# Kernel tuning notes

Hardware: AMD Instinct MI355X
Metric: run time of the kernel (lower is better)

The kernel has to match this reference:

```python
import jax, jax.numpy as jnp
import numpy as np

N_NODES = 50000
N_GRAPHS = 16
NEG_SLOPE = 0.2


def gat_layer(x, W, a_s, a_d, b, src, dst, num_nodes):
    # h: [N, out]
    h = x @ W
    # per-node attention logits (heads=1)
    al_s = (h * a_s).sum(-1)  # [N]
    al_d = (h * a_d).sum(-1)  # [N]
    e = jax.nn.leaky_relu(al_s[src] + al_d[dst], NEG_SLOPE)  # [E]
    # segment softmax over incoming edges of each destination node
    m = jax.ops.segment_max(e, dst, num_segments=num_nodes)
    p = jnp.exp(e - m[dst])
    z = jax.ops.segment_sum(p, dst, num_segments=num_nodes)
    coef = p / z[dst]  # self-loops guarantee z > 0
    out = jax.ops.segment_sum(coef[:, None] * h[src], dst, num_segments=num_nodes)
    return out + b


def setup_inputs() -> dict:
    key = jax.random.key(0)
    ks = jax.random.split(key, 20)
    in_dim, hid, out_dim = 256, 128, 128
    E = 800000
    x = jax.random.normal(ks[0], (N_NODES, in_dim), dtype=jnp.float32)
    edge_index = jax.random.randint(ks[1], (2, E), 0, N_NODES, dtype=jnp.int32)
    batch = jnp.sort(jax.random.randint(ks[2], (N_NODES,), 0, N_GRAPHS, dtype=jnp.int32))

    def glorot(k, shape):
        fan = shape[0] + shape[-1]
        s = jnp.sqrt(6.0 / fan)
        return jax.random.uniform(k, shape, jnp.float32, -s, s)

    dims = [(in_dim, hid), (hid, hid), (hid, out_dim)]
    inp = {"x": x, "edge_index": edge_index, "batch": batch}
    for i, (di, do) in enumerate(dims):
        inp[f"W{i}"] = glorot(ks[3 + 4 * i], (di, do))
        inp[f"as{i}"] = glorot(ks[4 + 4 * i], (1, do))[0]
        inp[f"ad{i}"] = glorot(ks[5 + 4 * i], (1, do))[0]
        inp[f"b{i}"] = jnp.zeros((do,), jnp.float32)
    return inp


def reference(x, edge_index, batch, W0, as0, ad0, b0, W1, as1, ad1, b1, W2, as2, ad2, b2):
    # add self loops once (PyG GATConv add_self_loops=True)
    loops = jnp.arange(N_NODES, dtype=edge_index.dtype)
    src = jnp.concatenate([edge_index[0], loops])
    dst = jnp.concatenate([edge_index[1], loops])

    h = gat_layer(x, W0, as0, ad0, b0, src, dst, N_NODES)
    h = jax.nn.relu(h)  # act; dropout is identity at eval
    h = gat_layer(h, W1, as1, ad1, b1, src, dst, N_NODES)
    h = jax.nn.relu(h)
    node_emb = gat_layer(h, W2, as2, ad2, b2, src, dst, N_NODES)

    # global_mean_pool
    b32 = batch.astype(jnp.int32)
    sums = jax.ops.segment_sum(node_emb, b32, num_segments=N_GRAPHS)
    cnt = jax.ops.segment_sum(jnp.ones((N_NODES,), node_emb.dtype), b32, num_segments=N_GRAPHS)
    return sums / jnp.maximum(cnt, 1.0)[:, None]
```

## Files before the change

### kernel.cpp

```cpp
#include <hip/hip_runtime.h>
#include <math.h>

#define NN 50000
#define NE 800000
#define NTE (NE + NN)
#define NG 16
#define HID 128
#define NEG_SLOPE 0.2f

#define NBUK 391
#define SLOT 2560
#define EPW 4096
#define NWG_E ((NTE + EPW - 1) / EPW)
#define GEMM_GRID ((NN + 63) / 64)

#define BPAD 136
#define SMEM_BYTES 34816

typedef __attribute__((ext_vector_type(8))) __bf16 bf16x8;
typedef __attribute__((ext_vector_type(4))) float f32x4;

union V16 {
    float4 f4;
    uint4 u4;
    bf16x8 b8;
    __bf16 h[8];
};

__global__ void k_prep(int* __restrict__ bwr, float* __restrict__ sums,
                       int* __restrict__ off,
                       const float* __restrict__ W0, const float* __restrict__ W1,
                       const float* __restrict__ W2, __bf16* __restrict__ Wt0,
                       __bf16* __restrict__ Wt1, __bf16* __restrict__ Wt2) {
    int t = blockIdx.x * blockDim.x + threadIdx.x;
    if (t == 0) off[NN] = NTE;
    if (t <= NBUK) bwr[t] = 0;
    if (t < NG * HID) sums[t] = 0.0f;
    if (t < 256 * HID) {
        int k = t >> 7, n = t & 127;
        Wt0[(size_t)n * 256 + k] = (__bf16)W0[t];
    } else if (t < 256 * HID + HID * HID) {
        int u = t - 256 * HID;
        int k = u >> 7, n = u & 127;
        Wt1[(size_t)n * HID + k] = (__bf16)W1[u];
    } else if (t < 256 * HID + 2 * HID * HID) {
        int u = t - 256 * HID - HID * HID;
        int k = u >> 7, n = u & 127;
        Wt2[(size_t)n * HID + k] = (__bf16)W2[u];
    }
}

__device__ __forceinline__ void scatter_body(const int* __restrict__ ei,
                                             int* __restrict__ bwr,
                                             int* __restrict__ rec, int blk,
                                             char* smem) {
    int* hist = (int*)smem;
    int* cur = hist + NBUK;
    int t = threadIdx.x;
    for (int b = t; b < NBUK; b += 256) hist[b] = 0;
    __syncthreads();
    int base = blk * EPW;
    #pragma unroll
    for (int r = 0; r < EPW / 256; r++) {
        int idx = base + r * 256 + t;
        if (idx < NTE) {
            int dst = (idx < NE) ? ei[NE + idx] : (idx - NE);
            atomicAdd(&hist[dst >> 7], 1);
        }
    }
    __syncthreads();
    for (int b = t; b < NBUK; b += 256) {
        int c = hist[b];
        if (c) cur[b] = atomicAdd(&bwr[b], c);
    }
    __syncthreads();
    #pragma unroll
    for (int r = 0; r < EPW / 256; r++) {
        int idx = base + r * 256 + t;
        if (idx < NTE) {
            int src, dst;
            if (idx < NE) { src = ei[idx]; dst = ei[NE + idx]; }
            else          { src = idx - NE; dst = src; }
            int b = dst >> 7;
            int pos = atomicAdd(&cur[b], 1);
            rec[(size_t)b * SLOT + pos] = src | ((dst & 127) << 17);
        }
    }
}

__device__ __forceinline__ void scan512(const int* __restrict__ bwr, int* s) {
    int t = threadIdx.x;
    s[t] = (t < NBUK) ? bwr[t] : 0;
    s[t + 256] = (t + 256 < NBUK) ? bwr[t + 256] : 0;
    __syncthreads();
    for (int o = 1; o < 512; o <<= 1) {
        int a0 = (t >= o) ? s[t - o] : 0;
        int a1 = s[t + 256 - o];
        __syncthreads();
        s[t] += a0;
        s[t + 256] += a1;
        __syncthreads();
    }
}

__global__ __launch_bounds__(256) void k_bfill(const int* __restrict__ bwr,
                                               const int* __restrict__ rec,
                                               int* __restrict__ off,
                                               int* __restrict__ csr) {
    __shared__ int s[512];
    __shared__ int cnt[128];
    __shared__ int scn[128];
    __shared__ int cur[128];
    int b = blockIdx.x, t = threadIdx.x;
    scan512(bwr, s);
    int base = s[b] - bwr[b];
    int n = bwr[b];
    const int* rb = rec + (size_t)b * SLOT;
    if (t < 128) cnt[t] = 0;
    __syncthreads();
    for (int i = t; i < n; i += 256) atomicAdd(&cnt[rb[i] >> 17], 1);
    __syncthreads();
    if (t < 128) scn[t] = cnt[t];
    __syncthreads();
    #pragma unroll
    for (int o = 1; o < 128; o <<= 1) {
        int add = (t >= o && t < 128) ? scn[t - o] : 0;
        __syncthreads();
        if (t < 128) scn[t] += add;
        __syncthreads();
    }
    if (t < 128) {
        int ex = scn[t] - cnt[t];
        cur[t] = ex;
        int d = b * 128 + t;
        if (d < NN) off[d] = base + ex;
    }
    __syncthreads();
    for (int i = t; i < n; i += 256) {
        int r = rb[i];
        int dloc = r >> 17;
        int src = r & 131071;
        int pos = atomicAdd(&cur[dloc], 1);
        csr[base + pos] = src;
    }
}

template <typename AT, int K>
__device__ __forceinline__ void gemm_body(const AT* __restrict__ A,
                                          const __bf16* __restrict__ Bt,
                                          __bf16* __restrict__ C,
                                          const float* __restrict__ a_s,
                                          const float* __restrict__ a_d,
                                          float* __restrict__ als,
                                          float* __restrict__ ald,
                                          int M, int blk, char* smem) {
    __bf16(*Bs)[BPAD] = (__bf16(*)[BPAD])smem;

    int tid = threadIdx.x;
    int rowBase = blk * 64;
    int wv = tid >> 6;
    int lane = tid & 63;
    int g = lane >> 4;
    int c = lane & 15;

    int rowA = rowBase + wv * 16 + c;
    bool va = rowA < M;

    f32x4 acc[8];
    #pragma unroll
    for (int ni = 0; ni < 8; ni++) acc[ni] = (f32x4){0.f, 0.f, 0.f, 0.f};

    for (int kh = 0; kh < K; kh += 128) {
        if (kh) __syncthreads();
        #pragma unroll
        for (int rep = 0; rep < 8; rep++) {
            int ch = rep * 256 + tid;
            int r = ch >> 4, q = ch & 15;
            *(float4*)&Bs[r][q * 8] = *(const float4*)(Bt + (size_t)r * K + kh + q * 8);
        }
        bf16x8 afr[4];
        #pragma unroll
        for (int kc = 0; kc < 4; kc++) {
            if constexpr (sizeof(AT) == 2) {
                V16 t;
                t.f4 = (float4){0.f, 0.f, 0.f, 0.f};
                if (va) t.f4 = *(const float4*)((const __bf16*)A + (size_t)rowA * K + kh + kc * 32 + g * 8);
                afr[kc] = t.b8;
            } else {
                float vv[8] = {0.f, 0.f, 0.f, 0.f, 0.f, 0.f, 0.f, 0.f};
                if (va) {
                    const float* Ap = (const float*)A + (size_t)rowA * K + kh + kc * 32 + g * 8;
                    float4 v0 = *(const float4*)Ap;
                    float4 v1 = *(const float4*)(Ap + 4);
                    vv[0] = v0.x; vv[1] = v0.y; vv[2] = v0.z; vv[3] = v0.w;
                    vv[4] = v1.x; vv[5] = v1.y; vv[6] = v1.z; vv[7] = v1.w;
                }
                V16 t;
                #pragma unroll
                for (int q = 0; q < 8; q++) t.h[q] = (__bf16)vv[q];
                afr[kc] = t.b8;
            }
        }
        __syncthreads();

        #pragma unroll
        for (int kc = 0; kc < 4; kc++) {
            #pragma unroll
            for (int ni = 0; ni < 8; ni++) {
                bf16x8 b = *(const bf16x8*)&Bs[ni * 16 + c][kc * 32 + g * 8];
                acc[ni] = __builtin_amdgcn_mfma_f32_16x16x32_bf16(afr[kc], b, acc[ni], 0, 0, 0);
            }
        }
    }

    float asv[8], adv[8];
    #pragma unroll
    for (int ni = 0; ni < 8; ni++) {
        asv[ni] = a_s[ni * 16 + c];
        adv[ni] = a_d[ni * 16 + c];
    }
    int rb = rowBase + wv * 16 + g * 4;
    #pragma unroll
    for (int i = 0; i < 4; i++) {
        int row = rb + i;
        float s = 0.f, dd = 0.f;
        #pragma unroll
        for (int ni = 0; ni < 8; ni++) {
            float v = acc[ni][i];
            s = fmaf(v, asv[ni], s);
            dd = fmaf(v, adv[ni], dd);
        }
        #pragma unroll
        for (int o = 1; o <= 8; o <<= 1) {
            s += __shfl_xor(s, o);
            dd += __shfl_xor(dd, o);
        }
        if (row < M) {
            #pragma unroll
            for (int ni = 0; ni < 8; ni++)
                C[(size_t)row * HID + ni * 16 + c] = (__bf16)acc[ni][i];
            if (c == 0) {
                als[row] = s;
                ald[row] = dd;
            }
        }
    }
}

__global__ __launch_bounds__(256, 4) void k_gemm_bf16(const __bf16* __restrict__ A,
                                                      const __bf16* __restrict__ Bt,
                                                      __bf16* __restrict__ C,
                                                      const float* __restrict__ a_s,
                                                      const float* __restrict__ a_d,
                                                      float* __restrict__ als,
                                                      float* __restrict__ ald) {
    __shared__ __align__(16) char smem[SMEM_BYTES];
    gemm_body<__bf16, HID>(A, Bt, C, a_s, a_d, als, ald, NN, blockIdx.x, smem);
}

__global__ __launch_bounds__(256, 4) void k_gemm0_scatter(const float* __restrict__ x,
                                                          const __bf16* __restrict__ Wt0,
                                                          __bf16* __restrict__ C,
                                                          const float* __restrict__ a_s,
                                                          const float* __restrict__ a_d,
                                                          float* __restrict__ als,
                                                          float* __restrict__ ald,
                                                          const int* __restrict__ ei,
                                                          int* __restrict__ bwr,
                                                          int* __restrict__ rec) {
    __shared__ __align__(16) char smem[SMEM_BYTES];
    if (blockIdx.x < GEMM_GRID) {
        gemm_body<float, 256>(x, Wt0, C, a_s, a_d, als, ald, NN, blockIdx.x, smem);
    } else {
        scatter_body(ei, bwr, rec, blockIdx.x - GEMM_GRID, smem);
    }
}

__global__ __launch_bounds__(256) void k_attn(const __bf16* __restrict__ h,
                                              const float* __restrict__ als,
                                              const float* __restrict__ ald,
                                              const int* __restrict__ off,
                                              const int* __restrict__ csr,
                                              const float* __restrict__ bias,
                                              __bf16* __restrict__ yout,
                                              int do_relu) {
    __shared__ int2 s_e[4][64];
    int gt = blockIdx.x * blockDim.x + threadIdx.x;
    int d = gt >> 6;
    int lane = gt & 63;
    if (d >= NN) return;
    int wv = threadIdx.x >> 6;
    int grp = lane >> 4;
    int c = lane & 15;

    int e0 = off[d], e1 = off[d + 1];
    int deg = e1 - e0;
    float ald_d = ald[d];
    float acc[8] = {0.f, 0.f, 0.f, 0.f, 0.f, 0.f, 0.f, 0.f};

    if (deg <= 64) {
        int s = 0;
        float e = -INFINITY;
        if (lane < deg) {
            s = csr[e0 + lane];
            float t = als[s] + ald_d;
            e = (t > 0.0f) ? t : NEG_SLOPE * t;
        }
        float mx = e;
        #pragma unroll
        for (int o = 32; o > 0; o >>= 1) mx = fmaxf(mx, __shfl_xor(mx, o));
        float p = (lane < deg) ? __expf(e - mx) : 0.0f;
        float z = p;
        #pragma unroll
        for (int o = 32; o > 0; o >>= 1) z += __shfl_xor(z, o);
        float inv_z = 1.0f / z;
        s_e[wv][lane] = make_int2(s, __float_as_int(p * inv_z));

        int degR = (deg + 3) & ~3;
        #pragma unroll 4
        for (int k = grp; k < degR; k += 4) {
            int2 pr = s_e[wv][k];
            int ss = pr.x;
            float cf = __int_as_float(pr.y);
            V16 v;
            v.f4 = *(const float4*)(h + (size_t)ss * HID + c * 8);
            #pragma unroll
            for (int i = 0; i < 4; i++) {
                unsigned int u = (&v.u4.x)[i];
                float lo = __uint_as_float(u << 16);
                float hi = __uint_as_float(u & 0xffff0000u);
                acc[2 * i]     = fmaf(cf, lo, acc[2 * i]);
                acc[2 * i + 1] = fmaf(cf, hi, acc[2 * i + 1]);
            }
        }
    } else {
        float mx = -INFINITY;
        for (int j = e0 + lane; j < e1; j += 64) {
            float t = als[csr[j]] + ald_d;
            t = (t > 0.0f) ? t : NEG_SLOPE * t;
            mx = fmaxf(mx, t);
        }
        #pragma unroll
        for (int o = 32; o > 0; o >>= 1) mx = fmaxf(mx, __shfl_xor(mx, o));
        float z = 0.0f;
        for (int j = e0 + lane; j < e1; j += 64) {
            float t = als[csr[j]] + ald_d;
            t = (t > 0.0f) ? t : NEG_SLOPE * t;
            z += __expf(t - mx);
        }
        #pragma unroll
        for (int o = 32; o > 0; o >>= 1) z += __shfl_xor(z, o);
        float inv_z = 1.0f / z;
        for (int k = grp; k < deg; k += 4) {
            int ss = csr[e0 + k];
            float t = als[ss] + ald_d;
            t = (t > 0.0f) ? t : NEG_SLOPE * t;
            float cf = __expf(t - mx) * inv_z;
            V16 v;
            v.f4 = *(const float4*)(h + (size_t)ss * HID + c * 8);
            #pragma unroll
            for (int i = 0; i < 4; i++) {
                unsigned int u = (&v.u4.x)[i];
                float lo = __uint_as_float(u << 16);
                float hi = __uint_as_float(u & 0xffff0000u);
                acc[2 * i]     = fmaf(cf, lo, acc[2 * i]);
                acc[2 * i + 1] = fmaf(cf, hi, acc[2 * i + 1]);
            }
        }
    }

    #pragma unroll
    for (int t = 0; t < 8; t++) {
        acc[t] += __shfl_xor(acc[t], 16);
        acc[t] += __shfl_xor(acc[t], 32);
    }

    if (grp == 0) {
        float4 b0 = *(const float4*)(bias + c * 8);
        float4 b1 = *(const float4*)(bias + c * 8 + 4);
        acc[0] += b0.x; acc[1] += b0.y; acc[2] += b0.z; acc[3] += b0.w;
        acc[4] += b1.x; acc[5] += b1.y; acc[6] += b1.z; acc[7] += b1.w;
        if (do_relu) {
            #pragma unroll
            for (int t = 0; t < 8; t++) acc[t] = fmaxf(acc[t], 0.0f);
        }
        V16 o;
        #pragma unroll
        for (int t = 0; t < 8; t++) o.h[t] = (__bf16)acc[t];
        *(float4*)(yout + (size_t)d * HID + c * 8) = o.f4;
    }
}

__global__ void k_pool(const __bf16* __restrict__ emb, const int* __restrict__ batch,
                       float* __restrict__ sums) {
    int t = threadIdx.x;
    int base = blockIdx.x * 64;
    int end = base + 64;
    if (end > NN) end = NN;
    float acc = 0.0f;
    int g_cur = -1;
    for (int n = base; n < end; ++n) {
        int g = batch[n];
        if (g != g_cur) {
            if (g_cur >= 0) atomicAdd(&sums[g_cur * HID + t], acc);
            acc = 0.0f;
            g_cur = g;
        }
        acc += (float)emb[(size_t)n * HID + t];
    }
    if (g_cur >= 0) atomicAdd(&sums[g_cur * HID + t], acc);
}

__global__ void k_div(const float* __restrict__ sums, const int* __restrict__ batch,
                      float* __restrict__ out) {
    int i = blockIdx.x * blockDim.x + threadIdx.x;
    if (i >= NG * HID) return;
    int g = i >> 7;
    int lo = 0, hi = NN;
    while (lo < hi) { int mid = (lo + hi) >> 1; if (batch[mid] < g) lo = mid + 1; else hi = mid; }
    int lo2 = lo, hi2 = NN;
    while (lo2 < hi2) { int mid = (lo2 + hi2) >> 1; if (batch[mid] < g + 1) lo2 = mid + 1; else hi2 = mid; }
    int c = lo2 - lo;
    out[i] = sums[i] / (float)(c > 1 ? c : 1);
}

extern "C" void kernel_launch(void* const* d_in, const int* in_sizes, int n_in,
                              void* d_out, int out_size, void* d_ws, size_t ws_size,
                              hipStream_t stream) {
    const float* x     = (const float*)d_in[0];
    const int*   ei    = (const int*)d_in[1];
    const int*   batch = (const int*)d_in[2];
    const float* W[3]  = {(const float*)d_in[3], (const float*)d_in[7], (const float*)d_in[11]};
    const float* AS[3] = {(const float*)d_in[4], (const float*)d_in[8], (const float*)d_in[12]};
    const float* AD[3] = {(const float*)d_in[5], (const float*)d_in[9], (const float*)d_in[13]};
    const float* BI[3] = {(const float*)d_in[6], (const float*)d_in[10], (const float*)d_in[14]};
    float* out = (float*)d_out;

    char* ws = (char*)d_ws;
    size_t o = 0;
    auto alloc = [&](size_t bytes) {
        void* p = ws + o;
        o = (o + bytes + 255) & ~(size_t)255;
        return p;
    };
    __bf16* hb  = (__bf16*)alloc((size_t)NN * HID * 2);
    __bf16* yb  = (__bf16*)alloc((size_t)NN * HID * 2);
    __bf16* Wt0 = (__bf16*)alloc((size_t)256 * HID * 2);
    __bf16* Wt1 = (__bf16*)alloc((size_t)HID * HID * 2);
    __bf16* Wt2 = (__bf16*)alloc((size_t)HID * HID * 2);
    float* als  = (float*)alloc(NN * 4);
    float* ald  = (float*)alloc(NN * 4);
    int* off    = (int*)alloc((NN + 1) * 4);
    int* bwr    = (int*)alloc((NBUK + 1) * 4);
    int* rec    = (int*)alloc((size_t)NBUK * SLOT * 4);
    int* csr    = (int*)alloc((size_t)NTE * 4);
    float* sums = (float*)alloc(NG * HID * 4);
    (void)ws_size; (void)in_sizes; (void)n_in; (void)out_size;

    const int wave_grid = (NN * 64 + 255) / 256;

    k_prep<<<(256 * HID + 2 * HID * HID + 255) / 256, 256, 0, stream>>>(
        bwr, sums, off, W[0], W[1], W[2], Wt0, Wt1, Wt2);

    k_gemm0_scatter<<<GEMM_GRID + NWG_E, 256, 0, stream>>>(
        x, Wt0, hb, AS[0], AD[0], als, ald, ei, bwr, rec);

    k_bfill<<<NBUK, 256, 0, stream>>>(bwr, rec, off, csr);

    k_attn<<<wave_grid, 256, 0, stream>>>(hb, als, ald, off, csr, BI[0], yb, 1);

    k_gemm_bf16<<<GEMM_GRID, 256, 0, stream>>>(yb, Wt1, hb, AS[1], AD[1], als, ald);
    k_attn<<<wave_grid, 256, 0, stream>>>(hb, als, ald, off, csr, BI[1], yb, 1);

    k_gemm_bf16<<<GEMM_GRID, 256, 0, stream>>>(yb, Wt2, hb, AS[2], AD[2], als, ald);
    k_attn<<<wave_grid, 256, 0, stream>>>(hb, als, ald, off, csr, BI[2], yb, 0);

    k_pool<<<(NN + 63) / 64, 128, 0, stream>>>(yb, batch, sums);
    k_div<<<(NG * HID + 255) / 256, 256, 0, stream>>>(sums, batch, out);
}
```

Measured before the change: 296.1 us.

## Process two nodes per wave in attention and fuse mean-pool into last layer

The attention kernel now gives each 32-lane half-wave its own destination node. Each half-wave keeps 2 edge groups instead of 4, and the LDS staging of source indices and coefficients is replaced by register shuffles. The final layer accumulates node embeddings per graph in shared memory and issues atomics straight away, which removes the separate pool kernel and the round-trip through global memory of the last embedding. The cost is less memory-level parallelism per node (2 gathers in flight instead of 4) and a block-wide sync in the pooling path. The grid size assumes NN divides evenly, which holds for 50000.

```diff
diff --git a/kernel.cpp b/kernel.cpp
--- a/kernel.cpp
+++ b/kernel.cpp
@@ -283,45 +283,48 @@
                                               const int* __restrict__ csr,
                                               const float* __restrict__ bias,
                                               __bf16* __restrict__ yout,
-                                              int do_relu) {
-    __shared__ int2 s_e[4][64];
-    int gt = blockIdx.x * blockDim.x + threadIdx.x;
-    int d = gt >> 6;
-    int lane = gt & 63;
-    if (d >= NN) return;
-    int wv = threadIdx.x >> 6;
-    int grp = lane >> 4;
+                                              const int* __restrict__ batch,
+                                              float* __restrict__ sums,
+                                              int do_relu, int do_pool) {
+    __shared__ float py[8][128];
+    __shared__ int pg[8];
+    int tid = threadIdx.x;
+    int w = (blockIdx.x * blockDim.x + tid) >> 6;
+    int lane = tid & 63;
+    int half = lane >> 5;
+    int l32 = lane & 31;
+    int gn = (lane >> 4) & 1;
     int c = lane & 15;
+    int d = 2 * w + half;
 
     int e0 = off[d], e1 = off[d + 1];
     int deg = e1 - e0;
     float ald_d = ald[d];
     float acc[8] = {0.f, 0.f, 0.f, 0.f, 0.f, 0.f, 0.f, 0.f};
 
-    if (deg <= 64) {
+    if (deg <= 32) {
         int s = 0;
         float e = -INFINITY;
-        if (lane < deg) {
-            s = csr[e0 + lane];
+        if (l32 < deg) {
+            s = csr[e0 + l32];
             float t = als[s] + ald_d;
             e = (t > 0.0f) ? t : NEG_SLOPE * t;
         }
         float mx = e;
         #pragma unroll
-        for (int o = 32; o > 0; o >>= 1) mx = fmaxf(mx, __shfl_xor(mx, o));
-        float p = (lane < deg) ? __expf(e - mx) : 0.0f;
+        for (int o = 16; o > 0; o >>= 1) mx = fmaxf(mx, __shfl_xor(mx, o));
+        float p = (l32 < deg) ? __expf(e - mx) : 0.0f;
         float z = p;
         #pragma unroll
-        for (int o = 32; o > 0; o >>= 1) z += __shfl_xor(z, o);
-        float inv_z = 1.0f / z;
-        s_e[wv][lane] = make_int2(s, __float_as_int(p * inv_z));
-
-        int degR = (deg + 3) & ~3;
+        for (int o = 16; o > 0; o >>= 1) z += __shfl_xor(z, o);
+        float cf = p * (1.0f / z);
+
+        int degR = (deg + 1) & ~1;
         #pragma unroll 4
-        for (int k = grp; k < degR; k += 4) {
-            int2 pr = s_e[wv][k];
-            int ss = pr.x;
-            float cf = __int_as_float(pr.y);
+        for (int k = gn; k < degR; k += 2) {
+            int srcl = (half << 5) + k;
+            int ss = __shfl(s, srcl);
+            float cw = __shfl(cf, srcl);
             V16 v;
             v.f4 = *(const float4*)(h + (size_t)ss * HID + c * 8);
             #pragma unroll
@@ -329,33 +332,33 @@
                 unsigned int u = (&v.u4.x)[i];
                 float lo = __uint_as_float(u << 16);
                 float hi = __uint_as_float(u & 0xffff0000u);
-                acc[2 * i]     = fmaf(cf, lo, acc[2 * i]);
-                acc[2 * i + 1] = fmaf(cf, hi, acc[2 * i + 1]);
+                acc[2 * i]     = fmaf(cw, lo, acc[2 * i]);
+                acc[2 * i + 1] = fmaf(cw, hi, acc[2 * i + 1]);
             }
         }
     } else {
         float mx = -INFINITY;
-        for (int j = e0 + lane; j < e1; j += 64) {
+        for (int j = e0 + l32; j < e1; j += 32) {
             float t = als[csr[j]] + ald_d;
             t = (t > 0.0f) ? t : NEG_SLOPE * t;
             mx = fmaxf(mx, t);
         }
         #pragma unroll
-        for (int o = 32; o > 0; o >>= 1) mx = fmaxf(mx, __shfl_xor(mx, o));
+        for (int o = 16; o > 0; o >>= 1) mx = fmaxf(mx, __shfl_xor(mx, o));
         float z = 0.0f;
-        for (int j = e0 + lane; j < e1; j += 64) {
+        for (int j = e0 + l32; j < e1; j += 32) {
             float t = als[csr[j]] + ald_d;
             t = (t > 0.0f) ? t : NEG_SLOPE * t;
             z += __expf(t - mx);
         }
         #pragma unroll
-        for (int o = 32; o > 0; o >>= 1) z += __shfl_xor(z, o);
+        for (int o = 16; o > 0; o >>= 1) z += __shfl_xor(z, o);
         float inv_z = 1.0f / z;
-        for (int k = grp; k < deg; k += 4) {
+        for (int k = gn; k < deg; k += 2) {
             int ss = csr[e0 + k];
             float t = als[ss] + ald_d;
             t = (t > 0.0f) ? t : NEG_SLOPE * t;
-            float cf = __expf(t - mx) * inv_z;
+            float cw = __expf(t - mx) * inv_z;
             V16 v;
             v.f4 = *(const float4*)(h + (size_t)ss * HID + c * 8);
             #pragma unroll
@@ -363,19 +366,16 @@
                 unsigned int u = (&v.u4.x)[i];
                 float lo = __uint_as_float(u << 16);
                 float hi = __uint_as_float(u & 0xffff0000u);
-                acc[2 * i]     = fmaf(cf, lo, acc[2 * i]);
-                acc[2 * i + 1] = fmaf(cf, hi, acc[2 * i + 1]);
-            }
-        }
-    }
-
-    #pragma unroll
-    for (int t = 0; t < 8; t++) {
-        acc[t] += __shfl_xor(acc[t], 16);
-        acc[t] += __shfl_xor(acc[t], 32);
-    }
-
-    if (grp == 0) {
+                acc[2 * i]     = fmaf(cw, lo, acc[2 * i]);
+                acc[2 * i + 1] = fmaf(cw, hi, acc[2 * i + 1]);
+            }
+        }
+    }
+
+    #pragma unroll
+    for (int t = 0; t < 8; t++) acc[t] += __shfl_xor(acc[t], 16);
+
+    if (l32 < 16) {
         float4 b0 = *(const float4*)(bias + c * 8);
         float4 b1 = *(const float4*)(bias + c * 8 + 4);
         acc[0] += b0.x; acc[1] += b0.y; acc[2] += b0.z; acc[3] += b0.w;
@@ -384,31 +384,36 @@
             #pragma unroll
             for (int t = 0; t < 8; t++) acc[t] = fmaxf(acc[t], 0.0f);
         }
-        V16 o;
-        #pragma unroll
-        for (int t = 0; t < 8; t++) o.h[t] = (__bf16)acc[t];
-        *(float4*)(yout + (size_t)d * HID + c * 8) = o.f4;
-    }
-}
-
-__global__ void k_pool(const __bf16* __restrict__ emb, const int* __restrict__ batch,
-                       float* __restrict__ sums) {
-    int t = threadIdx.x;
-    int base = blockIdx.x * 64;
-    int end = base + 64;
-    if (end > NN) end = NN;
-    float acc = 0.0f;
-    int g_cur = -1;
-    for (int n = base; n < end; ++n) {
-        int g = batch[n];
-        if (g != g_cur) {
-            if (g_cur >= 0) atomicAdd(&sums[g_cur * HID + t], acc);
-            acc = 0.0f;
-            g_cur = g;
-        }
-        acc += (float)emb[(size_t)n * HID + t];
-    }
-    if (g_cur >= 0) atomicAdd(&sums[g_cur * HID + t], acc);
+        if (!do_pool) {
+            V16 o;
+            #pragma unroll
+            for (int t = 0; t < 8; t++) o.h[t] = (__bf16)acc[t];
+            *(float4*)(yout + (size_t)d * HID + c * 8) = o.f4;
+        } else {
+            int nib = (tid >> 6) * 2 + half;
+            #pragma unroll
+            for (int t = 0; t < 8; t++) py[nib][c * 8 + t] = acc[t];
+            if (c == 0) pg[nib] = batch[d];
+        }
+    }
+    if (do_pool) {
+        __syncthreads();
+        if (tid < 128) {
+            float a = 0.0f;
+            int gc = pg[0];
+            #pragma unroll
+            for (int n = 0; n < 8; n++) {
+                int g = pg[n];
+                if (g != gc) {
+                    atomicAdd(&sums[gc * HID + tid], a);
+                    a = 0.0f;
+                    gc = g;
+                }
+                a += py[n][tid];
+            }
+            atomicAdd(&sums[gc * HID + tid], a);
+        }
+    }
 }
 
 __global__ void k_div(const float* __restrict__ sums, const int* __restrict__ batch,
@@ -457,7 +462,7 @@
     float* sums = (float*)alloc(NG * HID * 4);
     (void)ws_size; (void)in_sizes; (void)n_in; (void)out_size;
 
-    const int wave_grid = (NN * 64 + 255) / 256;
+    const int attn_grid = (NN / 2) * 64 / 256;
 
     k_prep<<<(256 * HID + 2 * HID * HID + 255) / 256, 256, 0, stream>>>(
         bwr, sums, off, W[0], W[1], W[2], Wt0, Wt1, Wt2);
@@ -467,14 +472,16 @@
 
     k_bfill<<<NBUK, 256, 0, stream>>>(bwr, rec, off, csr);
 
-    k_attn<<<wave_grid, 256, 0, stream>>>(hb, als, ald, off, csr, BI[0], yb, 1);
+    k_attn<<<attn_grid, 256, 0, stream>>>(hb, als, ald, off, csr, BI[0], yb,
+                                          batch, sums, 1, 0);
 
     k_gemm_bf16<<<GEMM_GRID, 256, 0, stream>>>(yb, Wt1, hb, AS[1], AD[1], als, ald);
-    k_attn<<<wave_grid, 256, 0, stream>>>(hb, als, ald, off, csr, BI[1], yb, 1);
+    k_attn<<<attn_grid, 256, 0, stream>>>(hb, als, ald, off, csr, BI[1], yb,
+                                          batch, sums, 1, 0);
 
     k_gemm_bf16<<<GEMM_GRID, 256, 0, stream>>>(yb, Wt2, hb, AS[2], AD[2], als, ald);
-    k_attn<<<wave_grid, 256, 0, stream>>>(hb, als, ald, off, csr, BI[2], yb, 0);
-
-    k_pool<<<(NN + 63) / 64, 128, 0, stream>>>(yb, batch, sums);
+    k_attn<<<attn_grid, 256, 0, stream>>>(hb, als, ald, off, csr, BI[2], yb,
+                                          batch, sums, 0, 1);
+
     k_div<<<(NG * HID + 255) / 256, 256, 0, stream>>>(sums, batch, out);
 }
```

Result: slower. 309.7 us (+4.6%).
